# Optimization experiments

Measured on AMD Instinct MI355X. Metric: run time of the kernel, lower is better.

The kernel has to match this reference:

```python
import jax, jax.numpy as jnp
import numpy as np

B, L, H = 8192, 64, 128
DEPTH = 3
EPS = 1e-5


def setup_inputs() -> dict:
    key = jax.random.key(0)
    ks = jax.random.split(key, 1 + 6)
    hidden_states = jax.random.normal(ks[0], (B, L, H), dtype=jnp.float32)
    # stacked per-layer params: Linear(H,H) -> LayerNorm(H) -> ReLU -> Linear(H, H//2)
    s1 = 1.0 / np.sqrt(H)
    W1 = jax.random.uniform(ks[1], (DEPTH, H, H), jnp.float32, -s1, s1)
    b1 = jax.random.uniform(ks[2], (DEPTH, H), jnp.float32, -s1, s1)
    gamma = jnp.ones((DEPTH, H), jnp.float32)
    beta = jnp.zeros((DEPTH, H), jnp.float32)
    W2 = jax.random.uniform(ks[3], (DEPTH, H, H // 2), jnp.float32, -s1, s1)
    b2 = jax.random.uniform(ks[4], (DEPTH, H // 2), jnp.float32, -s1, s1)
    return {
        "hidden_states": hidden_states,
        "W1": W1, "b1": b1, "gamma": gamma, "beta": beta,
        "W2": W2, "b2": b2,
        "lengths": L,
    }


def _layernorm(x, g, b):
    mu = jnp.mean(x, axis=-1, keepdims=True)
    var = jnp.mean(jnp.square(x - mu), axis=-1, keepdims=True)
    return (x - mu) * jax.lax.rsqrt(var + EPS) * g + b


def reference(hidden_states, W1, b1, gamma, beta, W2, b2, lengths):
    # hidden_states: [B, L, H]; max(lengths) == L
    x = hidden_states
    for i in range(DEPTH):
        h = jnp.einsum('blh,hk->blk', x, W1[i]) + b1[i]          # [B, L, H]
        h = jax.nn.relu(_layernorm(h, gamma[i], beta[i]))
        x1 = jnp.einsum('blh,hk->blk', h, W2[i]) + b2[i]          # [B, L, H//2]
        x2 = jnp.max(x1, axis=1, keepdims=True)                   # max-pool over seq
        x2 = jnp.broadcast_to(x2, x1.shape)                       # repeat to L
        x = jnp.concatenate([x1, x2], axis=2)                     # [B, L, H]
    return jnp.max(x, axis=1)                                     # [B, H]
```

## Files before the change

kernel.cpp:

```cpp
#include <hip/hip_runtime.h>

#define NB 8192
#define NL 64
#define NH 128

typedef __bf16 bf16x8 __attribute__((ext_vector_type(8)));
typedef float f32x4 __attribute__((ext_vector_type(4)));
typedef float f32x2 __attribute__((ext_vector_type(2)));
typedef unsigned short ushort8 __attribute__((ext_vector_type(8)));

__device__ __host__ __forceinline__ int p2l(int p) {
  return (p & ~31) + ((p & 1) << 4) + ((p & 31) >> 1);
}
__device__ __host__ __forceinline__ int pi2(int p) {
  return (p & 1) ? 64 + (p >> 1) : (p >> 1);
}

__device__ __forceinline__ unsigned pk2(float lo, float hi) {
  union { __bf16 b[2]; unsigned u; } t;
  t.b[0] = (__bf16)lo; t.b[1] = (__bf16)hi;
  return t.u;
}

__global__ __launch_bounds__(256) void repack_w(const float* __restrict__ W1,
                                                const float* __restrict__ W2,
                                                const float* __restrict__ gamma,
                                                const float* __restrict__ beta,
                                                unsigned short* __restrict__ wp1,
                                                unsigned short* __restrict__ wp2,
                                                float* __restrict__ gbt) {
  int t = blockIdx.x * 256 + threadIdx.x;
  int lane = t & 63, g = t >> 6;
  if (g < 96) {
    int layer = g >> 5, rem = g & 31, nt = rem >> 2, ks = rem & 3;
    int n = nt * 16 + (lane & 15);
    int kb = ks * 32 + (lane >> 4) * 8;
    ushort8 v;
#pragma unroll
    for (int r = 0; r < 8; ++r) {
      int k = kb + r;
      int srck = (layer == 0) ? k : pi2(k);
      union { __bf16 b; unsigned short u; } c;
      c.b = (__bf16)W1[(layer * 128 + srck) * 128 + n];
      v[r] = c.u;
    }
    *reinterpret_cast<ushort8*>(wp1 + ((size_t)g * 64 + lane) * 8) = v;
  } else if (g < 144) {
    int g2 = g - 96;
    int layer = g2 >> 4, rem = g2 & 15, nt = rem >> 2, ks = rem & 3;
    int n = nt * 16 + (lane & 15);
    int kb = ks * 32 + (lane >> 4) * 8;
    ushort8 v;
#pragma unroll
    for (int r = 0; r < 8; ++r) {
      union { __bf16 b; unsigned short u; } c;
      c.b = (__bf16)W2[(layer * 128 + p2l(kb + r)) * 64 + n];
      v[r] = c.u;
    }
    *reinterpret_cast<ushort8*>(wp2 + ((size_t)g2 * 64 + lane) * 8) = v;
  } else if (g < 150) {
    int g2 = g - 144;
    int layer = g2 >> 1, param = g2 & 1;
    const float* src = (param == 0 ? gamma : beta) + layer * 128;
    float* dst = gbt + layer * 288 + param * 144;
    int p0 = lane * 2;
#pragma unroll
    for (int u = 0; u < 2; ++u) {
      int p = p0 + u;
      dst[(p >> 5) * 36 + (p & 31)] = src[p2l(p)];
    }
  }
}

__global__ __launch_bounds__(256) void fused_mlp(
    const float* __restrict__ hidden,
    const float* __restrict__ b1,
    const float* __restrict__ b2,
    const unsigned short* __restrict__ wp1u,
    const unsigned short* __restrict__ wp2u,
    const float* __restrict__ gbt,
    float* __restrict__ out) {
  __shared__ __align__(16) unsigned short xbuf[NL * NH];
  __shared__ __align__(16) float gbuf[864];

  const int tid = threadIdx.x;
  const int wave = tid >> 6, lane = tid & 63;
  const int ci = lane & 15, lg = lane >> 4;
  char* xc = reinterpret_cast<char*>(xbuf);

  const int abase = ci * 256;
  const int axor = (ci & 7) << 4;

  {
    if (tid < 96) {
#pragma unroll
      for (int u = 0; u < 9; ++u) gbuf[tid * 9 + u] = gbt[tid * 9 + u];
    }
  }

  const float* src = hidden + (size_t)blockIdx.x * (NL * NH);
#pragma unroll
  for (int i = 0; i < 4; ++i) {
    int f = i * 256 + tid;
    int row = f >> 4;
    int cb = (f & 15) * 16;
    const float4* p = reinterpret_cast<const float4*>(src + f * 8);
    float4 a = p[0], bq = p[1];
    bf16x8 v;
    v[0] = (__bf16)a.x;  v[1] = (__bf16)a.y;  v[2] = (__bf16)a.z;  v[3] = (__bf16)a.w;
    v[4] = (__bf16)bq.x; v[5] = (__bf16)bq.y; v[6] = (__bf16)bq.z; v[7] = (__bf16)bq.w;
    *reinterpret_cast<bf16x8*>(xc + row * 256 + (cb ^ ((row & 7) << 4))) = v;
  }
  __syncthreads();

  for (int layer = 0; layer < 3; ++layer) {
    const unsigned short* wl1 = wp1u + (size_t)layer * 16384;
    const float bv0 = b1[layer * 128 + wave * 32 + ci];
    const float bv1 = b1[layer * 128 + wave * 32 + 16 + ci];
    const int dby = (wave * 16 + ci) * 4;

    f32x4 acc[4][2];
#pragma unroll
    for (int mt = 0; mt < 4; ++mt) {
      acc[mt][0] = f32x4{bv0, bv0, bv0, bv0};
      acc[mt][1] = f32x4{bv1, bv1, bv1, bv1};
    }
#pragma unroll
    for (int ks = 0; ks < 4; ++ks) {
      bf16x8 bf0 = *reinterpret_cast<const bf16x8*>(
          wl1 + (((wave * 2 + 0) * 4 + ks) * 64 + lane) * 8);
      bf16x8 bf1 = *reinterpret_cast<const bf16x8*>(
          wl1 + (((wave * 2 + 1) * 4 + ks) * 64 + lane) * 8);
      int cbx = ((ks * 64 + lg * 16) ^ axor) + abase;
#pragma unroll
      for (int mt = 0; mt < 4; ++mt) {
        bf16x8 af = *reinterpret_cast<const bf16x8*>(xc + mt * 4096 + cbx);
        acc[mt][0] = __builtin_amdgcn_mfma_f32_16x16x32_bf16(af, bf0, acc[mt][0], 0, 0, 0);
        acc[mt][1] = __builtin_amdgcn_mfma_f32_16x16x32_bf16(af, bf1, acc[mt][1], 0, 0, 0);
      }
    }
    __syncthreads();

#pragma unroll
    for (int mt = 0; mt < 4; ++mt)
#pragma unroll
      for (int r = 0; r < 4; ++r) {
        int row = mt * 16 + lg * 4 + r;
        *reinterpret_cast<unsigned*>(
            xc + row * 256 + (dby ^ ((row & 7) << 4))) =
            pk2(acc[mt][0][r], acc[mt][1][r]);
      }
    __syncthreads();

    {
      const int row = wave * 16 + (lane >> 2);
      const int q = lane & 3;
      const int rb = row * 256, rx = (row & 7) << 4;
      bf16x8 h0 = *reinterpret_cast<const bf16x8*>(xc + rb + ((q * 64 + 0) ^ rx));
      bf16x8 h1 = *reinterpret_cast<const bf16x8*>(xc + rb + ((q * 64 + 16) ^ rx));
      bf16x8 h2 = *reinterpret_cast<const bf16x8*>(xc + rb + ((q * 64 + 32) ^ rx));
      bf16x8 h3 = *reinterpret_cast<const bf16x8*>(xc + rb + ((q * 64 + 48) ^ rx));
      f32x2 f[16];
#pragma unroll
      for (int cch = 0; cch < 4; ++cch) {
        bf16x8 hv = (cch == 0) ? h0 : (cch == 1) ? h1 : (cch == 2) ? h2 : h3;
#pragma unroll
        for (int j2 = 0; j2 < 4; ++j2)
          f[cch * 4 + j2] = f32x2{(float)hv[j2 * 2], (float)hv[j2 * 2 + 1]};
      }
      f32x2 s2 = {0.f, 0.f}, q2 = {0.f, 0.f};
#pragma unroll
      for (int i = 0; i < 16; ++i) { s2 += f[i]; q2 += f[i] * f[i]; }
      float s = s2.x + s2.y, sq = q2.x + q2.y;
      s += __shfl_xor(s, 1);  sq += __shfl_xor(sq, 1);
      s += __shfl_xor(s, 2);  sq += __shfl_xor(sq, 2);
      float mu = s * (1.f / 128.f);
      float var = sq * (1.f / 128.f) - mu * mu;
      float rs = rsqrtf(var + 1e-5f);
      const f32x2* gl = reinterpret_cast<const f32x2*>(gbuf + layer * 288 + q * 36);
      const f32x2* bl = reinterpret_cast<const f32x2*>(gbuf + layer * 288 + 144 + q * 36);
#pragma unroll
      for (int cch = 0; cch < 4; ++cch) {
        union { unsigned u[4]; bf16x8 v; } yy;
#pragma unroll
        for (int j2 = 0; j2 < 4; ++j2) {
          int i = cch * 4 + j2;
          f32x2 a2 = gl[i] * rs;
          f32x2 c2 = bl[i] - a2 * mu;
          f32x2 y2 = f[i] * a2 + c2;
          yy.u[j2] = pk2(fmaxf(y2.x, 0.f), fmaxf(y2.y, 0.f));
        }
        *reinterpret_cast<bf16x8*>(xc + rb + ((q * 64 + cch * 16) ^ rx)) = yy.v;
      }
    }
    __syncthreads();

    f32x4 acc2[4];
    {
      float b2v = b2[layer * 64 + wave * 16 + ci];
#pragma unroll
      for (int mt = 0; mt < 4; ++mt) acc2[mt] = f32x4{b2v, b2v, b2v, b2v};
    }
    const unsigned short* wl2 = wp2u + (size_t)layer * 8192;
#pragma unroll
    for (int ks = 0; ks < 4; ++ks) {
      bf16x8 bfr = *reinterpret_cast<const bf16x8*>(
          wl2 + ((wave * 4 + ks) * 64 + lane) * 8);
      int cbx = ((ks * 64 + lg * 16) ^ axor) + abase;
#pragma unroll
      for (int mt = 0; mt < 4; ++mt) {
        bf16x8 af = *reinterpret_cast<const bf16x8*>(xc + mt * 4096 + cbx);
        acc2[mt] = __builtin_amdgcn_mfma_f32_16x16x32_bf16(af, bfr, acc2[mt], 0, 0, 0);
      }
    }

    float mm;
    {
      float m = -3.0e38f;
#pragma unroll
      for (int mt = 0; mt < 4; ++mt)
#pragma unroll
        for (int r = 0; r < 4; ++r) m = fmaxf(m, acc2[mt][r]);
      m = fmaxf(m, __shfl_xor(m, 16));
      m = fmaxf(m, __shfl_xor(m, 32));
      mm = m;
    }

    if (layer < 2) {
      __syncthreads();
#pragma unroll
      for (int mt = 0; mt < 4; ++mt)
#pragma unroll
        for (int r = 0; r < 4; ++r) {
          int row = mt * 16 + lg * 4 + r;
          *reinterpret_cast<unsigned*>(
              xc + row * 256 + (dby ^ ((row & 7) << 4))) =
              pk2(acc2[mt][r], mm);
        }
      __syncthreads();
    } else {
      if (lg == 0) {
        size_t o = (size_t)blockIdx.x * 128 + wave * 16 + ci;
        out[o] = mm;
        out[o + 64] = mm;
      }
    }
  }
}

extern "C" void kernel_launch(void* const* d_in, const int* in_sizes, int n_in,
                              void* d_out, int out_size, void* d_ws, size_t ws_size,
                              hipStream_t stream) {
  const float* hidden = (const float*)d_in[0];
  const float* W1 = (const float*)d_in[1];
  const float* b1 = (const float*)d_in[2];
  const float* gamma = (const float*)d_in[3];
  const float* beta = (const float*)d_in[4];
  const float* W2 = (const float*)d_in[5];
  const float* b2 = (const float*)d_in[6];
  (void)in_sizes; (void)n_in; (void)out_size; (void)ws_size;

  unsigned short* wp1 = (unsigned short*)d_ws;
  unsigned short* wp2 = wp1 + 3 * 8 * 4 * 64 * 8;
  float* gbt = (float*)(wp2 + 3 * 4 * 4 * 64 * 8);
  float* out = (float*)d_out;

  repack_w<<<38, 256, 0, stream>>>(W1, W2, gamma, beta, wp1, wp2, gbt);
  fused_mlp<<<NB, 256, 0, stream>>>(hidden, b1, b2, wp1, wp2, gbt, out);
}
```

Before: 144.2 us.

## Double-buffer activations in LDS to drop barriers and widen swizzle

Splits the single LDS activation buffer into two ping-pong buffers: GEMM1 reads xA and writes xB, and GEMM2 reads xB and writes back to xA. This removes the two barriers that previously guarded overwriting the shared buffer. The XOR swizzle widens from 8 to 16 rows to cut LDS bank conflicts. W2 fragments and the b2 bias are now loaded before the LayerNorm stage so their latency overlaps it. The cost is twice the LDS per block, about 32KB for activations, which may reduce occupancy.

```diff
diff --git a/kernel.cpp b/kernel.cpp
--- a/kernel.cpp
+++ b/kernel.cpp
@@ -80,22 +80,22 @@
     const unsigned short* __restrict__ wp2u,
     const float* __restrict__ gbt,
     float* __restrict__ out) {
-  __shared__ __align__(16) unsigned short xbuf[NL * NH];
+  __shared__ __align__(16) unsigned short xAu[NL * NH];
+  __shared__ __align__(16) unsigned short xBu[NL * NH];
   __shared__ __align__(16) float gbuf[864];
 
   const int tid = threadIdx.x;
   const int wave = tid >> 6, lane = tid & 63;
   const int ci = lane & 15, lg = lane >> 4;
-  char* xc = reinterpret_cast<char*>(xbuf);
+  char* xA = reinterpret_cast<char*>(xAu);
+  char* xB = reinterpret_cast<char*>(xBu);
 
   const int abase = ci * 256;
-  const int axor = (ci & 7) << 4;
-
-  {
-    if (tid < 96) {
-#pragma unroll
-      for (int u = 0; u < 9; ++u) gbuf[tid * 9 + u] = gbt[tid * 9 + u];
-    }
+  const int axor = ci << 4;
+
+  if (tid < 96) {
+#pragma unroll
+    for (int u = 0; u < 9; ++u) gbuf[tid * 9 + u] = gbt[tid * 9 + u];
   }
 
   const float* src = hidden + (size_t)blockIdx.x * (NL * NH);
@@ -109,7 +109,7 @@
     bf16x8 v;
     v[0] = (__bf16)a.x;  v[1] = (__bf16)a.y;  v[2] = (__bf16)a.z;  v[3] = (__bf16)a.w;
     v[4] = (__bf16)bq.x; v[5] = (__bf16)bq.y; v[6] = (__bf16)bq.z; v[7] = (__bf16)bq.w;
-    *reinterpret_cast<bf16x8*>(xc + row * 256 + (cb ^ ((row & 7) << 4))) = v;
+    *reinterpret_cast<bf16x8*>(xA + row * 256 + (cb ^ ((row & 15) << 4))) = v;
   }
   __syncthreads();
 
@@ -134,32 +134,38 @@
       int cbx = ((ks * 64 + lg * 16) ^ axor) + abase;
 #pragma unroll
       for (int mt = 0; mt < 4; ++mt) {
-        bf16x8 af = *reinterpret_cast<const bf16x8*>(xc + mt * 4096 + cbx);
+        bf16x8 af = *reinterpret_cast<const bf16x8*>(xA + mt * 4096 + cbx);
         acc[mt][0] = __builtin_amdgcn_mfma_f32_16x16x32_bf16(af, bf0, acc[mt][0], 0, 0, 0);
         acc[mt][1] = __builtin_amdgcn_mfma_f32_16x16x32_bf16(af, bf1, acc[mt][1], 0, 0, 0);
       }
     }
-    __syncthreads();
-
 #pragma unroll
     for (int mt = 0; mt < 4; ++mt)
 #pragma unroll
       for (int r = 0; r < 4; ++r) {
         int row = mt * 16 + lg * 4 + r;
         *reinterpret_cast<unsigned*>(
-            xc + row * 256 + (dby ^ ((row & 7) << 4))) =
+            xB + row * 256 + (dby ^ ((lg * 4 + r) << 4))) =
             pk2(acc[mt][0][r], acc[mt][1][r]);
       }
     __syncthreads();
+
+    const unsigned short* wl2 = wp2u + (size_t)layer * 8192;
+    bf16x8 w2f[4];
+#pragma unroll
+    for (int ks = 0; ks < 4; ++ks)
+      w2f[ks] = *reinterpret_cast<const bf16x8*>(
+          wl2 + ((wave * 4 + ks) * 64 + lane) * 8);
+    float b2v = b2[layer * 64 + wave * 16 + ci];
 
     {
       const int row = wave * 16 + (lane >> 2);
       const int q = lane & 3;
-      const int rb = row * 256, rx = (row & 7) << 4;
-      bf16x8 h0 = *reinterpret_cast<const bf16x8*>(xc + rb + ((q * 64 + 0) ^ rx));
-      bf16x8 h1 = *reinterpret_cast<const bf16x8*>(xc + rb + ((q * 64 + 16) ^ rx));
-      bf16x8 h2 = *reinterpret_cast<const bf16x8*>(xc + rb + ((q * 64 + 32) ^ rx));
-      bf16x8 h3 = *reinterpret_cast<const bf16x8*>(xc + rb + ((q * 64 + 48) ^ rx));
+      const int rb = row * 256, rx = (lane >> 2) << 4;
+      bf16x8 h0 = *reinterpret_cast<const bf16x8*>(xB + rb + ((q * 64 + 0) ^ rx));
+      bf16x8 h1 = *reinterpret_cast<const bf16x8*>(xB + rb + ((q * 64 + 16) ^ rx));
+      bf16x8 h2 = *reinterpret_cast<const bf16x8*>(xB + rb + ((q * 64 + 32) ^ rx));
+      bf16x8 h3 = *reinterpret_cast<const bf16x8*>(xB + rb + ((q * 64 + 48) ^ rx));
       f32x2 f[16];
 #pragma unroll
       for (int cch = 0; cch < 4; ++cch) {
@@ -190,27 +196,21 @@
           f32x2 y2 = f[i] * a2 + c2;
           yy.u[j2] = pk2(fmaxf(y2.x, 0.f), fmaxf(y2.y, 0.f));
         }
-        *reinterpret_cast<bf16x8*>(xc + rb + ((q * 64 + cch * 16) ^ rx)) = yy.v;
+        *reinterpret_cast<bf16x8*>(xB + rb + ((q * 64 + cch * 16) ^ rx)) = yy.v;
       }
     }
     __syncthreads();
 
     f32x4 acc2[4];
-    {
-      float b2v = b2[layer * 64 + wave * 16 + ci];
-#pragma unroll
-      for (int mt = 0; mt < 4; ++mt) acc2[mt] = f32x4{b2v, b2v, b2v, b2v};
-    }
-    const unsigned short* wl2 = wp2u + (size_t)layer * 8192;
+#pragma unroll
+    for (int mt = 0; mt < 4; ++mt) acc2[mt] = f32x4{b2v, b2v, b2v, b2v};
 #pragma unroll
     for (int ks = 0; ks < 4; ++ks) {
-      bf16x8 bfr = *reinterpret_cast<const bf16x8*>(
-          wl2 + ((wave * 4 + ks) * 64 + lane) * 8);
       int cbx = ((ks * 64 + lg * 16) ^ axor) + abase;
 #pragma unroll
       for (int mt = 0; mt < 4; ++mt) {
-        bf16x8 af = *reinterpret_cast<const bf16x8*>(xc + mt * 4096 + cbx);
-        acc2[mt] = __builtin_amdgcn_mfma_f32_16x16x32_bf16(af, bfr, acc2[mt], 0, 0, 0);
+        bf16x8 af = *reinterpret_cast<const bf16x8*>(xB + mt * 4096 + cbx);
+        acc2[mt] = __builtin_amdgcn_mfma_f32_16x16x32_bf16(af, w2f[ks], acc2[mt], 0, 0, 0);
       }
     }
 
@@ -227,14 +227,13 @@
     }
 
     if (layer < 2) {
-      __syncthreads();
 #pragma unroll
       for (int mt = 0; mt < 4; ++mt)
 #pragma unroll
         for (int r = 0; r < 4; ++r) {
           int row = mt * 16 + lg * 4 + r;
           *reinterpret_cast<unsigned*>(
-              xc + row * 256 + (dby ^ ((row & 7) << 4))) =
+              xA + row * 256 + (dby ^ ((lg * 4 + r) << 4))) =
               pk2(acc2[mt][r], mm);
         }
       __syncthreads();
```

Result: no change. 142.0 us (-1.5%).
